# Optimization experiments

Measured on AMD Instinct MI355X. Metric: run time of the kernel, lower is better.

Reference implementation:

```python
import jax, jax.numpy as jnp
import numpy as np

IMG = 12
SIZE = 100000
ACC_SCALE = 255.0     # accurate_dft scale
APX_SCALE = 65536.0   # mod_scale for mult index 1 (in {1,2,4,10,11})


def _dft_mat():
    # scipy.linalg.dft(12): W[j,k] = exp(-2*pi*i*j*k/12); module adds 1e-5
    j = np.arange(IMG)
    W = np.exp(-2j * np.pi * np.outer(j, j) / IMG)
    return W.real + 1e-5, W.imag + 1e-5


def setup_inputs() -> dict:
    key = jax.random.key(0)
    x = jax.random.uniform(key, (1, SIZE, IMG, IMG), dtype=jnp.float32) * 255.0
    re, im = _dft_mat()
    wr = jnp.asarray(re.reshape(1, IMG * IMG), dtype=jnp.float32)
    wi = jnp.asarray(im.reshape(1, IMG * IMG), dtype=jnp.float32)
    return {"input": x, "weight_real": wr, "weight_imag": wi}


def _dft_pass(wr_flat, wi_flat, x, scale, rounded):
    # x: (size, 12, 12); wr_flat/wi_flat: (144,)
    rw = wr_flat.reshape(IMG, IMG)
    iw = wi_flat.reshape(IMG, IMG)
    if rounded:  # approx_dft quantizes weights to integers in [-(scale-1), scale-1]
        rw = jnp.round(rw * (scale - 1.0))
        iw = jnp.round(iw * (scale - 1.0))
    else:        # accurate_dft just scales
        rw = rw * scale
        iw = iw * scale
    # approx_matmul's tile/elementwise-mul/group-sum is exactly W @ x[i] per batch
    rt = jnp.matmul(rw, x) / scale          # (size,12,12)
    it = jnp.matmul(iw, x) / scale
    ro = (jnp.matmul(rt, rw) - jnp.matmul(it, iw)) / scale
    io = (jnp.matmul(rt, iw) + jnp.matmul(it, rw)) / scale
    return jnp.sqrt(ro * ro + io * io)      # |re + i*im|


def reference(input, weight_real, weight_imag):
    x = input[:, :, :IMG, :IMG][0]  # (size,12,12)
    acc = _dft_pass(weight_real[0], weight_imag[0], x, ACC_SCALE, False)
    apx = _dft_pass(weight_real[0], weight_imag[0], x, APX_SCALE, True)
    # torch `x.data = x_data` -> straight-through: value = approx, grad via accurate
    out = acc + jax.lax.stop_gradient(apx - acc)
    # output layout [len(mult_list)=1, 1, size, 12, 12]
    return out[None, None]
```

## Files before the change

### kernel.cpp

```cpp
#include <hip/hip_runtime.h>

#define IMG  12
#define NPIX 144
#define THREADS 64

__device__ __forceinline__ float rfl(float v) {
    return __builtin_bit_cast(float, __builtin_amdgcn_readfirstlane(__builtin_bit_cast(int, v)));
}

__global__ __launch_bounds__(THREADS, 2)
void dft_apx_kernel(const float* __restrict__ x,
                    const float* __restrict__ wr,
                    const float* __restrict__ wi,
                    float* __restrict__ out, int size)
{
    __shared__ float wqc[NPIX], wqs[NPIX];

    const int tid = threadIdx.x;
    for (int t = tid; t < NPIX; t += THREADS) {
        const int r = t / IMG, j = t - r * IMG;
        const int m = (r * j) % IMG;
        wqc[t] = rintf(wr[IMG + m] * 65535.0f);
        wqs[t] = rintf(wi[IMG + m] * 65535.0f);
    }
    __syncthreads();

    float cq[12], sq[12];
    #pragma unroll
    for (int m = 0; m < 12; ++m) {
        cq[m] = rfl(rintf(wr[IMG + m] * 65535.0f));
        sq[m] = rfl(rintf(wi[IMG + m] * 65535.0f));
    }

    const int img = blockIdx.x * THREADS + tid;
    if (img >= size) return;

    float X[NPIX];
    const float4* xg = (const float4*)(x + (size_t)img * NPIX);
    #pragma unroll
    for (int k = 0; k < NPIX / 4; ++k) {
        const float4 v = xg[k];
        X[4*k+0] = v.x; X[4*k+1] = v.y; X[4*k+2] = v.z; X[4*k+3] = v.w;
    }

    float* og = out + (size_t)img * NPIX;
    const float inv32 = 2.3283064365386963e-10f;

    #pragma unroll 1
    for (int r = 0; r < IMG; ++r) {
        float cr[12], sr[12];
        #pragma unroll
        for (int q = 0; q < 3; ++q) {
            const float4 a = *(const float4*)&wqc[r * IMG + 4*q];
            const float4 b = *(const float4*)&wqs[r * IMG + 4*q];
            cr[4*q+0]=a.x; cr[4*q+1]=a.y; cr[4*q+2]=a.z; cr[4*q+3]=a.w;
            sr[4*q+0]=b.x; sr[4*q+1]=b.y; sr[4*q+2]=b.z; sr[4*q+3]=b.w;
        }
        float rt[12], it[12];
        #pragma unroll
        for (int c = 0; c < 12; ++c) {
            float a = 0.0f, b = 0.0f;
            #pragma unroll
            for (int j = 0; j < 12; ++j) {
                a = fmaf(cr[j], X[j*12 + c], a);
                b = fmaf(sr[j], X[j*12 + c], b);
            }
            rt[c] = a; it[c] = b;
        }
        float o[12];
        #pragma unroll
        for (int c = 0; c < 12; ++c) {
            float ro = 0.0f, io = 0.0f;
            #pragma unroll
            for (int j = 0; j < 12; ++j) {
                const int m = (j * c) % 12;
                ro = fmaf(rt[j],  cq[m], ro);
                ro = fmaf(-it[j], sq[m], ro);
                io = fmaf(rt[j],  sq[m], io);
                io = fmaf(it[j],  cq[m], io);
            }
            o[c] = __builtin_amdgcn_sqrtf(fmaf(ro, ro, io * io)) * inv32;
        }
        float4* orow = (float4*)(og + r * IMG);
        orow[0] = make_float4(o[0], o[1], o[2],  o[3]);
        orow[1] = make_float4(o[4], o[5], o[6],  o[7]);
        orow[2] = make_float4(o[8], o[9], o[10], o[11]);
    }
}

extern "C" void kernel_launch(void* const* d_in, const int* in_sizes, int n_in,
                              void* d_out, int out_size, void* d_ws, size_t ws_size,
                              hipStream_t stream) {
    const float* x  = (const float*)d_in[0];
    const float* wr = (const float*)d_in[1];
    const float* wi = (const float*)d_in[2];
    float* out = (float*)d_out;

    const int size = in_sizes[0] / NPIX;
    const int blocks = (size + THREADS - 1) / THREADS;
    dft_apx_kernel<<<blocks, THREADS, 0, stream>>>(x, wr, wi, out, size);
}
```

Measured before the change: 131.1 us.

## Assign one output row per thread instead of one image per thread

Each thread now computes a single output row of one image instead of looping over all 12 rows, so the grid has 12x more threads, with 256-thread blocks. Each thread reads the whole 12x12 input image with float4 loads, so every image is loaded by 12 threads and the reuse depends on the cache. In exchange, per-thread register pressure drops sharply because the 144-float image array is gone, which should raise occupancy and latency hiding. The setup code now fills shared memory with a single guarded pass and the barrier moves after the broadcast weight loads.

```diff
diff --git a/kernel.cpp b/kernel.cpp
--- a/kernel.cpp
+++ b/kernel.cpp
@@ -2,13 +2,13 @@
 
 #define IMG  12
 #define NPIX 144
-#define THREADS 64
+#define THREADS 256
 
 __device__ __forceinline__ float rfl(float v) {
     return __builtin_bit_cast(float, __builtin_amdgcn_readfirstlane(__builtin_bit_cast(int, v)));
 }
 
-__global__ __launch_bounds__(THREADS, 2)
+__global__ __launch_bounds__(THREADS, 4)
 void dft_apx_kernel(const float* __restrict__ x,
                     const float* __restrict__ wr,
                     const float* __restrict__ wi,
@@ -17,13 +17,12 @@
     __shared__ float wqc[NPIX], wqs[NPIX];
 
     const int tid = threadIdx.x;
-    for (int t = tid; t < NPIX; t += THREADS) {
-        const int r = t / IMG, j = t - r * IMG;
+    if (tid < NPIX) {
+        const int r = tid / IMG, j = tid - r * IMG;
         const int m = (r * j) % IMG;
-        wqc[t] = rintf(wr[IMG + m] * 65535.0f);
-        wqs[t] = rintf(wi[IMG + m] * 65535.0f);
+        wqc[tid] = rintf(wr[IMG + m] * 65535.0f);
+        wqs[tid] = rintf(wi[IMG + m] * 65535.0f);
     }
-    __syncthreads();
 
     float cq[12], sq[12];
     #pragma unroll
@@ -31,61 +30,59 @@
         cq[m] = rfl(rintf(wr[IMG + m] * 65535.0f));
         sq[m] = rfl(rintf(wi[IMG + m] * 65535.0f));
     }
+    __syncthreads();
 
-    const int img = blockIdx.x * THREADS + tid;
+    const int g   = blockIdx.x * THREADS + tid;
+    const int img = g / IMG;
+    const int r   = g - img * IMG;
     if (img >= size) return;
 
-    float X[NPIX];
-    const float4* xg = (const float4*)(x + (size_t)img * NPIX);
+    float cr[12], sr[12];
     #pragma unroll
-    for (int k = 0; k < NPIX / 4; ++k) {
-        const float4 v = xg[k];
-        X[4*k+0] = v.x; X[4*k+1] = v.y; X[4*k+2] = v.z; X[4*k+3] = v.w;
+    for (int q = 0; q < 3; ++q) {
+        const float4 a = *(const float4*)&wqc[r * IMG + 4*q];
+        const float4 b = *(const float4*)&wqs[r * IMG + 4*q];
+        cr[4*q+0]=a.x; cr[4*q+1]=a.y; cr[4*q+2]=a.z; cr[4*q+3]=a.w;
+        sr[4*q+0]=b.x; sr[4*q+1]=b.y; sr[4*q+2]=b.z; sr[4*q+3]=b.w;
     }
 
-    float* og = out + (size_t)img * NPIX;
-    const float inv32 = 2.3283064365386963e-10f;
-
-    #pragma unroll 1
-    for (int r = 0; r < IMG; ++r) {
-        float cr[12], sr[12];
-        #pragma unroll
-        for (int q = 0; q < 3; ++q) {
-            const float4 a = *(const float4*)&wqc[r * IMG + 4*q];
-            const float4 b = *(const float4*)&wqs[r * IMG + 4*q];
-            cr[4*q+0]=a.x; cr[4*q+1]=a.y; cr[4*q+2]=a.z; cr[4*q+3]=a.w;
-            sr[4*q+0]=b.x; sr[4*q+1]=b.y; sr[4*q+2]=b.z; sr[4*q+3]=b.w;
-        }
-        float rt[12], it[12];
+    const float* xim = x + (size_t)img * NPIX;
+    float rt[12] = {0,0,0,0,0,0,0,0,0,0,0,0};
+    float it[12] = {0,0,0,0,0,0,0,0,0,0,0,0};
+    #pragma unroll
+    for (int j = 0; j < 12; ++j) {
+        const float4 v0 = *(const float4*)(xim + j * IMG + 0);
+        const float4 v1 = *(const float4*)(xim + j * IMG + 4);
+        const float4 v2 = *(const float4*)(xim + j * IMG + 8);
+        const float xv[12] = {v0.x,v0.y,v0.z,v0.w, v1.x,v1.y,v1.z,v1.w, v2.x,v2.y,v2.z,v2.w};
+        const float wc = cr[j], ws = sr[j];
         #pragma unroll
         for (int c = 0; c < 12; ++c) {
-            float a = 0.0f, b = 0.0f;
-            #pragma unroll
-            for (int j = 0; j < 12; ++j) {
-                a = fmaf(cr[j], X[j*12 + c], a);
-                b = fmaf(sr[j], X[j*12 + c], b);
-            }
-            rt[c] = a; it[c] = b;
+            rt[c] = fmaf(wc, xv[c], rt[c]);
+            it[c] = fmaf(ws, xv[c], it[c]);
         }
-        float o[12];
+    }
+
+    const float inv32 = 2.3283064365386963e-10f;
+    float o[12];
+    #pragma unroll
+    for (int c = 0; c < 12; ++c) {
+        float ro = 0.0f, io = 0.0f;
         #pragma unroll
-        for (int c = 0; c < 12; ++c) {
-            float ro = 0.0f, io = 0.0f;
-            #pragma unroll
-            for (int j = 0; j < 12; ++j) {
-                const int m = (j * c) % 12;
-                ro = fmaf(rt[j],  cq[m], ro);
-                ro = fmaf(-it[j], sq[m], ro);
-                io = fmaf(rt[j],  sq[m], io);
-                io = fmaf(it[j],  cq[m], io);
-            }
-            o[c] = __builtin_amdgcn_sqrtf(fmaf(ro, ro, io * io)) * inv32;
+        for (int j = 0; j < 12; ++j) {
+            const int m = (j * c) % 12;
+            ro = fmaf(rt[j],  cq[m], ro);
+            ro = fmaf(-it[j], sq[m], ro);
+            io = fmaf(rt[j],  sq[m], io);
+            io = fmaf(it[j],  cq[m], io);
         }
-        float4* orow = (float4*)(og + r * IMG);
-        orow[0] = make_float4(o[0], o[1], o[2],  o[3]);
-        orow[1] = make_float4(o[4], o[5], o[6],  o[7]);
-        orow[2] = make_float4(o[8], o[9], o[10], o[11]);
+        o[c] = __builtin_amdgcn_sqrtf(fmaf(ro, ro, io * io)) * inv32;
     }
+
+    float4* orow = (float4*)(out + (size_t)img * NPIX + r * IMG);
+    orow[0] = make_float4(o[0], o[1], o[2],  o[3]);
+    orow[1] = make_float4(o[4], o[5], o[6],  o[7]);
+    orow[2] = make_float4(o[8], o[9], o[10], o[11]);
 }
 
 extern "C" void kernel_launch(void* const* d_in, const int* in_sizes, int n_in,
@@ -97,6 +94,7 @@
     float* out = (float*)d_out;
 
     const int size = in_sizes[0] / NPIX;
-    const int blocks = (size + THREADS - 1) / THREADS;
+    const int threads_total = size * IMG;
+    const int blocks = (threads_total + THREADS - 1) / THREADS;
     dft_apx_kernel<<<blocks, THREADS, 0, stream>>>(x, wr, wi, out, size);
 }
```

After: 132.1 us. About the same (+0.8%).
